# Performance work log

Measured on AMD Instinct MI355X. Metric: run time of the kernel, lower is better.

## Reference

```python
import jax, jax.numpy as jnp
import numpy as np

N = 8192
IN_F = 128
OUT_F = 64
ALPHA = 0.2  # LeakyReLU negative slope
EDGE_P = 0.02  # adjacency density
NEG_INF = -1e12


def setup_inputs() -> dict:
    key = jax.random.key(0)
    k1, k2, k3, k4 = jax.random.split(key, 4)
    input_h = jax.random.normal(k1, (N, IN_F), dtype=jnp.float32)
    # sparse-ish 0/1 adjacency mask, with self-loops so every softmax row is valid
    adj = (jax.random.uniform(k2, (N, N)) < EDGE_P).astype(jnp.float32)
    adj = adj + jnp.eye(N, dtype=jnp.float32)
    # xavier_uniform with gain 1.414 as in the torch init
    def xavier(k, shape, gain=1.414):
        fan_in, fan_out = shape[0], shape[1]
        bound = gain * np.sqrt(6.0 / (fan_in + fan_out))
        return jax.random.uniform(k, shape, jnp.float32, -bound, bound)
    W = xavier(k3, (IN_F, OUT_F))
    a = xavier(k4, (2 * OUT_F, 1))
    return {"input_h": input_h, "adj": adj, "W": W, "a": a}


def reference(input_h, adj, W, a):
    # Wh: [N, F]
    Wh = input_h @ W
    # e[i, j] = leakyrelu(a1 . Wh_i + a2 . Wh_j)  (decomposed, no N*N*2F concat)
    a1 = a[:OUT_F, 0]   # [F]
    a2 = a[OUT_F:, 0]   # [F]
    s_src = Wh @ a1     # [N]
    s_dst = Wh @ a2     # [N]
    e = jax.nn.leaky_relu(s_src[:, None] + s_dst[None, :], negative_slope=ALPHA)  # [N, N]
    att = jnp.where(adj > 0, e, NEG_INF)
    att = jax.nn.softmax(att, axis=1)
    # dropout is identity in eval mode (training=False)
    out_h = att @ Wh    # [N, F]
    return out_h
```

## Files before the change

### kernel.cpp

```cpp
#include <hip/hip_runtime.h>
#include <hip/hip_bf16.h>
#include <type_traits>

#define N 8192
#define IN_F 128
#define OUT_F 64
#define ALPHA 0.2f
#define LOG2E 1.442695040888963f

__device__ __forceinline__ float cvt(float x) { return x; }
__device__ __forceinline__ float cvt(__hip_bfloat16 x) { return __bfloat162float(x); }

__device__ __forceinline__ bool probe_fp32(const void* adj) {
    unsigned int u = *(const unsigned int*)adj;
    return (u == 0x3F800000u) || (u == 0x40000000u);
}

template <typename T>
__device__ __forceinline__ void k1_body(
    const T* __restrict__ h, const T* __restrict__ W, const T* __restrict__ a,
    float* __restrict__ Wh, float* __restrict__ s_src, float* __restrict__ s_dst,
    float* Wf, float (*hrow)[IN_F])
{
    const int tid  = threadIdx.x;
    const int w    = tid >> 6;
    const int lane = tid & 63;

    for (int idx = tid; idx < IN_F * OUT_F; idx += 256)
        Wf[idx] = cvt(W[idx]);

    const int row0 = blockIdx.x * 4;
    for (int idx = tid; idx < 4 * IN_F; idx += 256) {
        int r = idx >> 7, c = idx & (IN_F - 1);
        hrow[r][c] = cvt(h[(size_t)(row0 + r) * IN_F + c]);
    }
    __syncthreads();

    const int i = row0 + w;
    float acc = 0.f;
    #pragma unroll 8
    for (int t = 0; t < IN_F; ++t)
        acc = fmaf(hrow[w][t], Wf[t * OUT_F + lane], acc);

    Wh[(size_t)i * OUT_F + lane] = acc;

    float s1 = acc * cvt(a[lane]);
    float s2 = acc * cvt(a[OUT_F + lane]);
    #pragma unroll
    for (int off = 32; off; off >>= 1) {
        s1 += __shfl_xor(s1, off, 64);
        s2 += __shfl_xor(s2, off, 64);
    }
    if (lane == 0) { s_src[i] = s1; s_dst[i] = s2; }
}

__global__ __launch_bounds__(256) void gat_k1(
    const void* h, const void* W, const void* a, const void* adj,
    float* Wh, float* s_src, float* s_dst)
{
    __shared__ float Wf[IN_F * OUT_F];
    __shared__ float hrow[4][IN_F];
    if (probe_fp32(adj))
        k1_body<float>((const float*)h, (const float*)W, (const float*)a,
                       Wh, s_src, s_dst, Wf, hrow);
    else
        k1_body<__hip_bfloat16>((const __hip_bfloat16*)h, (const __hip_bfloat16*)W,
                                (const __hip_bfloat16*)a, Wh, s_src, s_dst, Wf, hrow);
}

template <typename TADJ, bool OUT_F32>
__device__ __forceinline__ void k2_body(
    const TADJ* __restrict__ adj, const float* __restrict__ Wh,
    const float* __restrict__ s_src, const float* __restrict__ s_dstg,
    void* __restrict__ outv, float2 (*pbuf)[512])
{
    const int tid  = threadIdx.x;
    const int w    = tid >> 6;
    const int lane = tid & 63;

    const int i = blockIdx.x * 4 + w;
    const float s_i = s_src[i];
    float2* buf = pbuf[w];

    float acc  = 0.f;
    float lsum = 0.f;

    for (int c = 0; c < 16; ++c) {
        const int jb = c * 512 + lane * 8;

        unsigned int bits[8];
        if constexpr (std::is_same<TADJ, float>::value) {
            const float* arow = adj + (size_t)i * N;
            const uint4 b0 = *((const uint4*)(arow + jb));
            const uint4 b1 = *((const uint4*)(arow + jb + 4));
            bits[0] = b0.x; bits[1] = b0.y; bits[2] = b0.z; bits[3] = b0.w;
            bits[4] = b1.x; bits[5] = b1.y; bits[6] = b1.z; bits[7] = b1.w;
        } else {
            const unsigned short* arow = (const unsigned short*)adj + (size_t)i * N;
            const uint4 a8 = *((const uint4*)(arow + jb));
            bits[0] = a8.x & 0xffffu; bits[1] = a8.x >> 16;
            bits[2] = a8.y & 0xffffu; bits[3] = a8.y >> 16;
            bits[4] = a8.z & 0xffffu; bits[5] = a8.z >> 16;
            bits[6] = a8.w & 0xffffu; bits[7] = a8.w >> 16;
        }

        const float4 sd0 = *((const float4*)(s_dstg + jb));
        const float4 sd1 = *((const float4*)(s_dstg + jb + 4));
        float sdv[8] = {sd0.x, sd0.y, sd0.z, sd0.w, sd1.x, sd1.y, sd1.z, sd1.w};

        float p[8];
        bool  nz[8];
        #pragma unroll
        for (int t = 0; t < 8; ++t) {
            float e = s_i + sdv[t];
            e = (e > 0.f) ? e : ALPHA * e;
            float pe = __builtin_exp2f(e * LOG2E);
            nz[t] = (bits[t] != 0u);
            p[t]  = nz[t] ? pe : 0.f;
            lsum += p[t];
        }

        int n = 0;
        #pragma unroll
        for (int t = 0; t < 8; ++t) {
            unsigned long long m = __ballot(nz[t]);
            if (nz[t]) {
                int pos = n + __popcll(m & ((1ull << lane) - 1ull));
                buf[pos] = make_float2(p[t], __int_as_float(jb + t));
            }
            n += (int)__popcll(m);
        }
        const int n4 = (n + 3) & ~3;
        if (lane < n4 - n) buf[n + lane] = make_float2(0.f, __int_as_float(0));
        __threadfence_block();

        for (int u0 = 0; u0 < n4; u0 += 4) {
            const float4 pa = *((const float4*)&buf[u0]);
            const float4 pb = *((const float4*)&buf[u0 + 2]);
            const int j0 = __float_as_int(pa.y), j1 = __float_as_int(pa.w);
            const int j2 = __float_as_int(pb.y), j3 = __float_as_int(pb.w);
            const float w0 = Wh[((size_t)j0 << 6) + lane];
            const float w1 = Wh[((size_t)j1 << 6) + lane];
            const float w2 = Wh[((size_t)j2 << 6) + lane];
            const float w3 = Wh[((size_t)j3 << 6) + lane];
            acc = fmaf(pa.x, w0, acc);
            acc = fmaf(pa.z, w1, acc);
            acc = fmaf(pb.x, w2, acc);
            acc = fmaf(pb.z, w3, acc);
        }
        __threadfence_block();
    }

    #pragma unroll
    for (int off = 32; off; off >>= 1)
        lsum += __shfl_xor(lsum, off, 64);

    const float v = acc / lsum;
    if constexpr (OUT_F32)
        ((float*)outv)[(size_t)i * OUT_F + lane] = v;
    else
        ((__hip_bfloat16*)outv)[(size_t)i * OUT_F + lane] = __float2bfloat16(v);
}

__global__ __launch_bounds__(256) void gat_k2(
    const void* adj, const float* Wh, const float* s_src, const float* s_dst,
    void* out)
{
    __shared__ __align__(16) float2 pbuf[4][512];
    if (probe_fp32(adj))
        k2_body<float, true>((const float*)adj, Wh, s_src, s_dst, out, pbuf);
    else
        k2_body<__hip_bfloat16, false>((const __hip_bfloat16*)adj, Wh, s_src, s_dst,
                                       out, pbuf);
}

extern "C" void kernel_launch(void* const* d_in, const int* in_sizes, int n_in,
                              void* d_out, int out_size, void* d_ws, size_t ws_size,
                              hipStream_t stream) {
    const void* h   = d_in[0];
    const void* adj = d_in[1];
    const void* W   = d_in[2];
    const void* a   = d_in[3];

    char* ws = (char*)d_ws;
    float* Wh    = (float*)ws;
    float* s_src = (float*)(ws + (size_t)N * OUT_F * 4);
    float* s_dst = s_src + N;

    gat_k1<<<N / 4, 256, 0, stream>>>(h, W, a, adj, Wh, s_src, s_dst);
    gat_k2<<<N / 4, 256, 0, stream>>>(adj, Wh, s_src, s_dst, d_out);
}
```

Baseline: 392.8 us.

## Replace sparse gather aggregation with dense bf16 MFMA over transposed Wh

The attention aggregation no longer compacts non-zero edges and gathers Wh rows per edge. It computes masked probabilities densely, packs them as bf16, and multiplies them with a transposed bf16 Wh using 16x16x32 MFMA instructions. Each block now handles 16 rows with 8 waves splitting the column range, and partial sums are reduced through shared memory. This removes per-edge ballot, compaction and scattered gathers in exchange for dense matrix work over all columns. Rounding both the probabilities and Wh to bf16 loses precision, and the transposed Wh stores in k1 are strided.

```diff
diff --git a/kernel.cpp b/kernel.cpp
--- a/kernel.cpp
+++ b/kernel.cpp
@@ -1,6 +1,5 @@
 #include <hip/hip_runtime.h>
 #include <hip/hip_bf16.h>
-#include <type_traits>
 
 #define N 8192
 #define IN_F 128
@@ -8,6 +7,9 @@
 #define ALPHA 0.2f
 #define LOG2E 1.442695040888963f
 
+typedef __attribute__((ext_vector_type(8))) short short8;
+typedef __attribute__((ext_vector_type(4))) float f32x4;
+
 __device__ __forceinline__ float cvt(float x) { return x; }
 __device__ __forceinline__ float cvt(__hip_bfloat16 x) { return __bfloat162float(x); }
 
@@ -16,162 +18,189 @@
     return (u == 0x3F800000u) || (u == 0x40000000u);
 }
 
+__device__ __forceinline__ short f2bf(float x) {
+    union { __hip_bfloat16 b; short s; } u;
+    u.b = __float2bfloat16(x);
+    return u.s;
+}
+__device__ __forceinline__ float bfbits2f(short s) {
+    union { unsigned int u; float f; } v;
+    v.u = ((unsigned int)(unsigned short)s) << 16;
+    return v.f;
+}
+
 template <typename T>
 __device__ __forceinline__ void k1_body(
     const T* __restrict__ h, const T* __restrict__ W, const T* __restrict__ a,
-    float* __restrict__ Wh, float* __restrict__ s_src, float* __restrict__ s_dst,
-    float* Wf, float (*hrow)[IN_F])
+    unsigned short* __restrict__ WhT, float* __restrict__ s_src, float* __restrict__ s_dst,
+    float (*WfT)[132], float (*hrow)[IN_F])
 {
     const int tid  = threadIdx.x;
     const int w    = tid >> 6;
     const int lane = tid & 63;
-
-    for (int idx = tid; idx < IN_F * OUT_F; idx += 256)
-        Wf[idx] = cvt(W[idx]);
-
-    const int row0 = blockIdx.x * 4;
-    for (int idx = tid; idx < 4 * IN_F; idx += 256) {
-        int r = idx >> 7, c = idx & (IN_F - 1);
-        hrow[r][c] = cvt(h[(size_t)(row0 + r) * IN_F + c]);
+    const int R0   = blockIdx.x * 16;
+
+    for (int idx = tid; idx < IN_F * OUT_F; idx += 256) {
+        int t = idx >> 6, f = idx & 63;
+        WfT[f][t] = cvt(W[idx]);
+    }
+    for (int idx = tid; idx < 16 * IN_F; idx += 256) {
+        int r = idx >> 7, c = idx & 127;
+        hrow[r][c] = cvt(h[(size_t)(R0 + r) * IN_F + c]);
     }
     __syncthreads();
 
-    const int i = row0 + w;
-    float acc = 0.f;
-    #pragma unroll 8
-    for (int t = 0; t < IN_F; ++t)
-        acc = fmaf(hrow[w][t], Wf[t * OUT_F + lane], acc);
-
-    Wh[(size_t)i * OUT_F + lane] = acc;
-
-    float s1 = acc * cvt(a[lane]);
-    float s2 = acc * cvt(a[OUT_F + lane]);
-    #pragma unroll
-    for (int off = 32; off; off >>= 1) {
-        s1 += __shfl_xor(s1, off, 64);
-        s2 += __shfl_xor(s2, off, 64);
-    }
-    if (lane == 0) { s_src[i] = s1; s_dst[i] = s2; }
+    const float a1 = cvt(a[lane]);
+    const float a2 = cvt(a[OUT_F + lane]);
+
+    for (int rr = 0; rr < 4; ++rr) {
+        const int rloc = w * 4 + rr;
+        const int i    = R0 + rloc;
+        float acc = 0.f;
+        #pragma unroll 8
+        for (int b = 0; b < 32; ++b) {
+            const float4 wv = *(const float4*)&WfT[lane][b * 4];
+            const float4 hv = *(const float4*)&hrow[rloc][b * 4];
+            acc = fmaf(hv.x, wv.x, acc);
+            acc = fmaf(hv.y, wv.y, acc);
+            acc = fmaf(hv.z, wv.z, acc);
+            acc = fmaf(hv.w, wv.w, acc);
+        }
+        WhT[(size_t)lane * N + i] = (unsigned short)f2bf(acc);
+
+        float s1 = acc * a1, s2 = acc * a2;
+        #pragma unroll
+        for (int off = 32; off; off >>= 1) {
+            s1 += __shfl_xor(s1, off, 64);
+            s2 += __shfl_xor(s2, off, 64);
+        }
+        if (lane == 0) { s_src[i] = s1; s_dst[i] = s2; }
+    }
 }
 
 __global__ __launch_bounds__(256) void gat_k1(
     const void* h, const void* W, const void* a, const void* adj,
-    float* Wh, float* s_src, float* s_dst)
-{
-    __shared__ float Wf[IN_F * OUT_F];
-    __shared__ float hrow[4][IN_F];
+    unsigned short* WhT, float* s_src, float* s_dst)
+{
+    __shared__ float WfT[OUT_F][132];
+    __shared__ float hrow[16][IN_F];
     if (probe_fp32(adj))
         k1_body<float>((const float*)h, (const float*)W, (const float*)a,
-                       Wh, s_src, s_dst, Wf, hrow);
+                       WhT, s_src, s_dst, WfT, hrow);
     else
         k1_body<__hip_bfloat16>((const __hip_bfloat16*)h, (const __hip_bfloat16*)W,
-                                (const __hip_bfloat16*)a, Wh, s_src, s_dst, Wf, hrow);
-}
-
+                                (const __hip_bfloat16*)a, WhT, s_src, s_dst, WfT, hrow);
+}
+
+#define K2_WAVES 8
 template <typename TADJ, bool OUT_F32>
 __device__ __forceinline__ void k2_body(
-    const TADJ* __restrict__ adj, const float* __restrict__ Wh,
-    const float* __restrict__ s_src, const float* __restrict__ s_dstg,
-    void* __restrict__ outv, float2 (*pbuf)[512])
+    const TADJ* __restrict__ adj,
+    const unsigned short* __restrict__ WhT,
+    const float* __restrict__ s_src,
+    const float* __restrict__ s_dst,
+    void* __restrict__ outv,
+    float (*Cpart)[16][65], float (*Lpart)[16])
 {
     const int tid  = threadIdx.x;
-    const int w    = tid >> 6;
+    const int wave = tid >> 6;
     const int lane = tid & 63;
-
-    const int i = blockIdx.x * 4 + w;
-    const float s_i = s_src[i];
-    float2* buf = pbuf[w];
-
-    float acc  = 0.f;
-    float lsum = 0.f;
-
-    for (int c = 0; c < 16; ++c) {
-        const int jb = c * 512 + lane * 8;
+    const int quad = lane >> 4;
+    const int l15  = lane & 15;
+    const int R0   = blockIdx.x * 16;
+
+    const int   row = R0 + l15;
+    const float si  = s_src[row];
+    const TADJ* __restrict__ arow = adj + (size_t)row * N;
+
+    f32x4 acc[4];
+    #pragma unroll
+    for (int nt = 0; nt < 4; ++nt) acc[nt] = (f32x4)0.f;
+    float ls = 0.f;
+
+    const int jw = wave * 1024;
+
+    for (int kt = 0; kt < 32; ++kt) {
+        const int jq = jw + kt * 32 + quad * 8;
 
         unsigned int bits[8];
-        if constexpr (std::is_same<TADJ, float>::value) {
-            const float* arow = adj + (size_t)i * N;
-            const uint4 b0 = *((const uint4*)(arow + jb));
-            const uint4 b1 = *((const uint4*)(arow + jb + 4));
+        if constexpr (sizeof(TADJ) == 4) {
+            const uint4 b0 = *(const uint4*)(arow + jq);
+            const uint4 b1 = *(const uint4*)(arow + jq + 4);
             bits[0] = b0.x; bits[1] = b0.y; bits[2] = b0.z; bits[3] = b0.w;
             bits[4] = b1.x; bits[5] = b1.y; bits[6] = b1.z; bits[7] = b1.w;
         } else {
-            const unsigned short* arow = (const unsigned short*)adj + (size_t)i * N;
-            const uint4 a8 = *((const uint4*)(arow + jb));
+            const uint4 a8 = *(const uint4*)(arow + jq);
             bits[0] = a8.x & 0xffffu; bits[1] = a8.x >> 16;
             bits[2] = a8.y & 0xffffu; bits[3] = a8.y >> 16;
             bits[4] = a8.z & 0xffffu; bits[5] = a8.z >> 16;
             bits[6] = a8.w & 0xffffu; bits[7] = a8.w >> 16;
         }
 
-        const float4 sd0 = *((const float4*)(s_dstg + jb));
-        const float4 sd1 = *((const float4*)(s_dstg + jb + 4));
-        float sdv[8] = {sd0.x, sd0.y, sd0.z, sd0.w, sd1.x, sd1.y, sd1.z, sd1.w};
-
-        float p[8];
-        bool  nz[8];
+        const float4 sd0 = *(const float4*)(s_dst + jq);
+        const float4 sd1 = *(const float4*)(s_dst + jq + 4);
+
+        short8 bfr[4];
+        #pragma unroll
+        for (int nt = 0; nt < 4; ++nt)
+            bfr[nt] = *(const short8*)(WhT + (size_t)(nt * 16 + l15) * N + jq);
+
+        const float sdv[8] = {sd0.x, sd0.y, sd0.z, sd0.w, sd1.x, sd1.y, sd1.z, sd1.w};
+
+        short8 A;
         #pragma unroll
         for (int t = 0; t < 8; ++t) {
-            float e = s_i + sdv[t];
-            e = (e > 0.f) ? e : ALPHA * e;
-            float pe = __builtin_exp2f(e * LOG2E);
-            nz[t] = (bits[t] != 0u);
-            p[t]  = nz[t] ? pe : 0.f;
-            lsum += p[t];
-        }
-
-        int n = 0;
-        #pragma unroll
-        for (int t = 0; t < 8; ++t) {
-            unsigned long long m = __ballot(nz[t]);
-            if (nz[t]) {
-                int pos = n + __popcll(m & ((1ull << lane) - 1ull));
-                buf[pos] = make_float2(p[t], __int_as_float(jb + t));
-            }
-            n += (int)__popcll(m);
-        }
-        const int n4 = (n + 3) & ~3;
-        if (lane < n4 - n) buf[n + lane] = make_float2(0.f, __int_as_float(0));
-        __threadfence_block();
-
-        for (int u0 = 0; u0 < n4; u0 += 4) {
-            const float4 pa = *((const float4*)&buf[u0]);
-            const float4 pb = *((const float4*)&buf[u0 + 2]);
-            const int j0 = __float_as_int(pa.y), j1 = __float_as_int(pa.w);
-            const int j2 = __float_as_int(pb.y), j3 = __float_as_int(pb.w);
-            const float w0 = Wh[((size_t)j0 << 6) + lane];
-            const float w1 = Wh[((size_t)j1 << 6) + lane];
-            const float w2 = Wh[((size_t)j2 << 6) + lane];
-            const float w3 = Wh[((size_t)j3 << 6) + lane];
-            acc = fmaf(pa.x, w0, acc);
-            acc = fmaf(pa.z, w1, acc);
-            acc = fmaf(pb.x, w2, acc);
-            acc = fmaf(pb.z, w3, acc);
-        }
-        __threadfence_block();
-    }
+            float e = si + sdv[t];
+            e = fmaxf(e, ALPHA * e);
+            float p = (bits[t] != 0u) ? __builtin_exp2f(e * LOG2E) : 0.f;
+            A[t] = f2bf(p);
+            ls += bfbits2f(A[t]);
+        }
+
+        #pragma unroll
+        for (int nt = 0; nt < 4; ++nt)
+            acc[nt] = __builtin_amdgcn_mfma_f32_16x16x32_bf16(A, bfr[nt], acc[nt], 0, 0, 0);
+    }
+
+    ls += __shfl_xor(ls, 16, 64);
+    ls += __shfl_xor(ls, 32, 64);
+    if (quad == 0) Lpart[wave][l15] = ls;
 
     #pragma unroll
-    for (int off = 32; off; off >>= 1)
-        lsum += __shfl_xor(lsum, off, 64);
-
-    const float v = acc / lsum;
-    if constexpr (OUT_F32)
-        ((float*)outv)[(size_t)i * OUT_F + lane] = v;
+    for (int nt = 0; nt < 4; ++nt)
+        #pragma unroll
+        for (int reg = 0; reg < 4; ++reg)
+            Cpart[wave][quad * 4 + reg][nt * 16 + l15] = acc[nt][reg];
+
+    __syncthreads();
+
+    for (int idx = tid; idx < 16 * OUT_F; idx += 512) {
+        const int i = idx >> 6, f = idx & 63;
+        float s = 0.f, l = 0.f;
+        #pragma unroll
+        for (int w = 0; w < K2_WAVES; ++w) {
+            s += Cpart[w][i][f];
+            l += Lpart[w][i];
+        }
+        const float v = s / l;
+        if constexpr (OUT_F32)
+            ((float*)outv)[(size_t)(R0 + i) * OUT_F + f] = v;
+        else
+            ((__hip_bfloat16*)outv)[(size_t)(R0 + i) * OUT_F + f] = __float2bfloat16(v);
+    }
+}
+
+__global__ __launch_bounds__(512) void gat_k2(
+    const void* adj, const unsigned short* WhT,
+    const float* s_src, const float* s_dst, void* out)
+{
+    __shared__ float Cpart[K2_WAVES][16][65];
+    __shared__ float Lpart[K2_WAVES][16];
+    if (probe_fp32(adj))
+        k2_body<float, true>((const float*)adj, WhT, s_src, s_dst, out, Cpart, Lpart);
     else
-        ((__hip_bfloat16*)outv)[(size_t)i * OUT_F + lane] = __float2bfloat16(v);
-}
-
-__global__ __launch_bounds__(256) void gat_k2(
-    const void* adj, const float* Wh, const float* s_src, const float* s_dst,
-    void* out)
-{
-    __shared__ __align__(16) float2 pbuf[4][512];
-    if (probe_fp32(adj))
-        k2_body<float, true>((const float*)adj, Wh, s_src, s_dst, out, pbuf);
-    else
-        k2_body<__hip_bfloat16, false>((const __hip_bfloat16*)adj, Wh, s_src, s_dst,
-                                       out, pbuf);
+        k2_body<unsigned short, false>((const unsigned short*)adj, WhT, s_src, s_dst,
+                                       out, Cpart, Lpart);
 }
 
 extern "C" void kernel_launch(void* const* d_in, const int* in_sizes, int n_in,
@@ -183,10 +212,10 @@
     const void* a   = d_in[3];
 
     char* ws = (char*)d_ws;
-    float* Wh    = (float*)ws;
-    float* s_src = (float*)(ws + (size_t)N * OUT_F * 4);
+    unsigned short* WhT = (unsigned short*)ws;
+    float* s_src = (float*)(ws + (size_t)OUT_F * N * 2);
     float* s_dst = s_src + N;
 
-    gat_k1<<<N / 4, 256, 0, stream>>>(h, W, a, adj, Wh, s_src, s_dst);
-    gat_k2<<<N / 4, 256, 0, stream>>>(adj, Wh, s_src, s_dst, d_out);
-}
+    gat_k1<<<N / 16, 256, 0, stream>>>(h, W, a, adj, WhT, s_src, s_dst);
+    gat_k2<<<N / 16, 512, 0, stream>>>(adj, WhT, s_src, s_dst, d_out);
+}
```

New measurement: 434.8 us. 10.7% more time.
